# Performance work log

Measured on AMD Instinct MI355X. Metric: run time of the kernel, lower is better.

## Reference

```python
import jax, jax.numpy as jnp
import numpy as np

D_STATE = 11
DT_RANK = 4
BN_EPS = 1e-5
RMS_EPS = 1e-5


def setup_inputs() -> dict:
    key = jax.random.key(0)
    ks = jax.random.split(key, 8)
    B, L, D = 8, 8192, 64
    x = jax.random.normal(ks[0], (B, L, D), dtype=jnp.float32)
    tconv_w = jax.random.normal(ks[1], (64, 1, 63), dtype=jnp.float32) * 0.1
    bn_gamma = jnp.ones((64,), jnp.float32)
    bn_beta = jnp.zeros((64,), jnp.float32)
    x_proj_weight = jax.random.normal(ks[2], (1, DT_RANK + 2 * D_STATE, 64), jnp.float32) * (64 ** -0.5)
    dt_projs_weight = jax.random.uniform(ks[3], (1, 64, DT_RANK), jnp.float32, -0.5, 0.5)
    # dt bias ~ inverse-softplus of dt in [1e-3, 1e-1]
    dt = jnp.exp(jax.random.uniform(ks[4], (1, 64), jnp.float32) * (np.log(0.1) - np.log(0.001)) + np.log(0.001))
    dt_projs_bias = dt + jnp.log(-jnp.expm1(-dt))
    A_logs = jnp.log(jnp.broadcast_to(jnp.arange(1, D_STATE + 1, dtype=jnp.float32), (64, D_STATE)))
    Ds = jnp.ones((64,), jnp.float32)
    rms_scale = jnp.ones((1, 64), jnp.float32)
    return {"x": x, "tconv_w": tconv_w, "bn_gamma": bn_gamma, "bn_beta": bn_beta,
            "x_proj_weight": x_proj_weight, "dt_projs_weight": dt_projs_weight,
            "dt_projs_bias": dt_projs_bias, "A_logs": A_logs, "Ds": Ds,
            "rms_scale": rms_scale}


def _silu(v):
    return v * jax.nn.sigmoid(v)


def reference(x, tconv_w, bn_gamma, bn_beta, x_proj_weight, dt_projs_weight,
              dt_projs_bias, A_logs, Ds, rms_scale):
    B, L, D = x.shape  # D == 64
    z = x
    xc = jnp.transpose(x, (0, 2, 1))  # (B, C, L)

    # depthwise conv1d, kernel 63, pad 31, no bias
    xc = jax.lax.conv_general_dilated(
        xc, tconv_w, window_strides=(1,), padding=[(31, 31)],
        feature_group_count=D, dimension_numbers=("NCH", "OIH", "NCH"))

    # BatchNorm1d (training-mode forward: batch stats, biased variance)
    mean = jnp.mean(xc, axis=(0, 2), keepdims=True)
    var = jnp.mean((xc - mean) ** 2, axis=(0, 2), keepdims=True)
    xc = (xc - mean) / jnp.sqrt(var + BN_EPS) * bn_gamma[None, :, None] + bn_beta[None, :, None]

    u = _silu(xc)  # (B, d_inner, L)

    # x_proj: (B,d,L) x (C,d) -> (B,C,L)
    x_dbl = jnp.einsum("bdl,cd->bcl", u, x_proj_weight[0])
    dts = x_dbl[:, :DT_RANK]                      # (B, r, L)
    Bs = x_dbl[:, DT_RANK:DT_RANK + D_STATE]      # (B, N, L)
    Cs = x_dbl[:, DT_RANK + D_STATE:]             # (B, N, L)

    dts = jnp.einsum("brl,dr->bdl", dts, dt_projs_weight[0])
    delta = jax.nn.softplus(dts + dt_projs_bias[0][None, :, None])  # (B,d,L)

    A = -jnp.exp(A_logs)  # (d, N)
    dA = jnp.exp(jnp.einsum("bdl,dn->lbdn", delta, A))      # (L,B,d,N)
    dBu = jnp.einsum("bdl,bnl->lbdn", delta * u, Bs)        # (L,B,d,N)

    def step(h, inp):
        dA_t, dBu_t = inp
        h = dA_t * h + dBu_t
        return h, h

    h0 = jnp.zeros((B, u.shape[1], D_STATE), dtype=u.dtype)
    _, hs = jax.lax.scan(step, h0, (dA, dBu))  # (L,B,d,N)

    y = jnp.einsum("lbdn,bnl->bdl", hs, Cs) + Ds[None, :, None] * u  # (B,d,L)

    y = jnp.transpose(y, (0, 2, 1))  # (B, L, d_inner)

    # RMSNorm
    ms = jnp.mean(y ** 2, axis=-1, keepdims=True)
    y = (rms_scale / jnp.sqrt(ms + RMS_EPS)) * y

    out = y * _silu(z)
    return out
```

## Files before the change

kernel.cpp:

```cpp
#include <hip/hip_runtime.h>
#include <hip/hip_bf16.h>
#include <hip/hip_fp16.h>
#include <math.h>

#define NB 8
#define LL 8192
#define DD 64
#define NS 11
#define NR 4
#define NC 512
#define LC (LL/NC)
#define CONV_LT 128
#define KW 63
#define PJ 64
#define NBKT 64
#define UH 72
#define WH 72

typedef _Float16 h2v __attribute__((ext_vector_type(2)));

__device__ __forceinline__ float sigmoidf_(float v){ return 1.f/(1.f+__expf(-v)); }
__device__ __forceinline__ float rnd16(float v){ return __half2float(__float2half_rn(v)); }

__global__ void k_zero(float* __restrict__ p){
  p[blockIdx.x*256 + threadIdx.x] = 0.f;
}

__global__ __launch_bounds__(512,4) void k_conv(const float* __restrict__ x,
                                              const float* __restrict__ w,
                                              __half* __restrict__ xc,
                                              __half* __restrict__ gate,
                                              float* __restrict__ bn_acc){
  const int b  = blockIdx.x / (LL/CONV_LT);
  const int lt = blockIdx.x % (LL/CONV_LT);
  const int l0 = lt*CONV_LT;
  __shared__ float xt[(CONV_LT+62)*DD];
  __shared__ float rs[512], rq[512];
  const int t = threadIdx.x;
  for (int i=t; i<(CONV_LT+62)*DD; i+=512){
    int lrel = i/DD, d = i%DD;
    int lg = l0 - 31 + lrel;
    xt[i] = (lg>=0 && lg<LL) ? x[((size_t)b*LL+lg)*DD + d] : 0.f;
  }
  __syncthreads();
  const int d = t & 63;
  const int base = (t >> 6) * 16;
  float acc[16];
  #pragma unroll
  for (int j=0;j<16;j++) acc[j]=0.f;
  #pragma unroll 1
  for (int kb=0; kb<4; ++kb){
    float wv[16];
    #pragma unroll
    for (int kk=0;kk<16;kk++){
      int k = kb*16+kk;
      wv[kk] = (k<KW) ? w[d*KW+k] : 0.f;
    }
    float xw[31];
    #pragma unroll
    for (int i=0;i<31;i++) xw[i] = xt[(base+kb*16+i)*DD + d];
    #pragma unroll
    for (int j=0;j<16;j++){
      #pragma unroll
      for (int kk=0;kk<16;kk++){
        acc[j] = fmaf(wv[kk], xw[j+kk], acc[j]);
      }
    }
  }
  float lsum=0.f, lsq=0.f;
  #pragma unroll
  for (int j=0;j<16;j++){
    size_t p = (size_t)b*LL + l0+base+j;
    xc[p*DD + d] = __float2half_rn(acc[j]);
    float z = xt[(base+j+31)*DD + d];
    gate[p*DD + d] = __float2half_rn(z * sigmoidf_(z));
    lsum += acc[j]; lsq = fmaf(acc[j],acc[j],lsq);
  }
  rs[t]=lsum; rq[t]=lsq;
  __syncthreads();
  if (t<64){
    float s=0.f, q=0.f;
    #pragma unroll
    for (int g=0; g<8; ++g){ s += rs[t+64*g]; q += rq[t+64*g]; }
    const int bkt = (blockIdx.x & (NBKT-1))*128;
    atomicAdd(&bn_acc[bkt+t],    s);
    atomicAdd(&bn_acc[bkt+64+t], q);
  }
}

__global__ __launch_bounds__(256,5) void k_proj(const __half* __restrict__ xc,
                                              const float* __restrict__ bn_acc,
                                              const float* __restrict__ gamma,
                                              const float* __restrict__ beta,
                                              const float* __restrict__ xpw,
                                              const float* __restrict__ dtw,
                                              const float* __restrict__ dtb,
                                              const float* __restrict__ Alog,
                                              __half2* __restrict__ duo,
                                              __half* __restrict__ bch,
                                              float* __restrict__ chunkst){
  const int b  = blockIdx.x / (LL/PJ);
  const int lt = blockIdx.x % (LL/PJ);
  const int l0 = lt*PJ;
  __shared__ __align__(16) _Float16 ulh[PJ*UH];
  __shared__ __align__(16) _Float16 wshh[26*WH];
  __shared__ float bcl[PJ][24];
  __shared__ float xd[PJ*NR];
  __shared__ float dtwsh[64*NR];
  __shared__ float bnred[2][4][64];
  const int t = threadIdx.x;
  for (int i=t; i<26*64; i+=256){ int c=i>>6, dd=i&63; wshh[c*WH+dd] = (_Float16)xpw[i]; }
  dtwsh[t] = dtw[t];
  if (t < 128){ bcl[t>>1][(t&1)?23:11] = 0.f; }
  const int d = t & 63, wv = t >> 6;
  {
    float ms=0.f, qs=0.f;
    #pragma unroll
    for (int k=wv*16; k<wv*16+16; ++k){
      ms += bn_acc[k*128 + d];
      qs += bn_acc[k*128 + 64 + d];
    }
    bnred[0][wv][d]=ms; bnred[1][wv][d]=qs;
  }
  __syncthreads();
  float msum = bnred[0][0][d]+bnred[0][1][d]+bnred[0][2][d]+bnred[0][3][d];
  float qsum = bnred[1][0][d]+bnred[1][1][d]+bnred[1][2][d]+bnred[1][3][d];
  const float inv_n = 1.f/((float)NB*(float)LL);
  float mean = msum*inv_n;
  float var  = qsum*inv_n - mean*mean;
  float sc = gamma[d] * rsqrtf(var + 1e-5f);
  float sh = beta[d] - mean*sc;
  float uu[16];
  #pragma unroll
  for (int j=0;j<16;j++){
    int lr = wv*16 + j;
    float v = __half2float(xc[((size_t)b*LL + l0+lr)*DD + d]);
    v = fmaf(v, sc, sh);
    _Float16 uh = (_Float16)(v * sigmoidf_(v));
    uu[j] = (float)uh;
    ulh[lr*UH+d] = uh;
  }
  __syncthreads();
  {
    const int cp  = t & 15;
    const int lrb = t >> 4;
    if (cp < 13){
      float acc0[4] = {0.f,0.f,0.f,0.f};
      float acc1[4] = {0.f,0.f,0.f,0.f};
      #pragma unroll 2
      for (int dd8=0; dd8<8; ++dd8){
        float4 w0v = *reinterpret_cast<const float4*>(&wshh[(2*cp  )*WH + dd8*8]);
        float4 w1v = *reinterpret_cast<const float4*>(&wshh[(2*cp+1)*WH + dd8*8]);
        const h2v* w0 = reinterpret_cast<const h2v*>(&w0v);
        const h2v* w1 = reinterpret_cast<const h2v*>(&w1v);
        #pragma unroll
        for (int p=0;p<4;p++){
          float4 uvv = *reinterpret_cast<const float4*>(&ulh[(lrb*4+p)*UH + dd8*8]);
          const h2v* up = reinterpret_cast<const h2v*>(&uvv);
#if __has_builtin(__builtin_amdgcn_fdot2)
          acc0[p] = __builtin_amdgcn_fdot2(w0[0], up[0], acc0[p], false);
          acc0[p] = __builtin_amdgcn_fdot2(w0[1], up[1], acc0[p], false);
          acc0[p] = __builtin_amdgcn_fdot2(w0[2], up[2], acc0[p], false);
          acc0[p] = __builtin_amdgcn_fdot2(w0[3], up[3], acc0[p], false);
          acc1[p] = __builtin_amdgcn_fdot2(w1[0], up[0], acc1[p], false);
          acc1[p] = __builtin_amdgcn_fdot2(w1[1], up[1], acc1[p], false);
          acc1[p] = __builtin_amdgcn_fdot2(w1[2], up[2], acc1[p], false);
          acc1[p] = __builtin_amdgcn_fdot2(w1[3], up[3], acc1[p], false);
#else
          #pragma unroll
          for (int q2=0;q2<4;q2++){
            acc0[p] += (float)w0[q2][0]*(float)up[q2][0] + (float)w0[q2][1]*(float)up[q2][1];
            acc1[p] += (float)w1[q2][0]*(float)up[q2][0] + (float)w1[q2][1]*(float)up[q2][1];
          }
#endif
        }
      }
      #pragma unroll
      for (int cc=0; cc<2; ++cc){
        int c = 2*cp+cc;
        #pragma unroll
        for (int p=0;p<4;p++){
          int lr = lrb*4+p;
          float v = cc ? acc1[p] : acc0[p];
          if (c < NR) xd[lr*NR+c] = v;
          else {
            int pos = c - NR;
            int slot = (pos < NS) ? pos : pos+1;
            bcl[lr][slot] = rnd16(v);
          }
        }
      }
    }
  }
  __syncthreads();
  {
    __half2* dst = reinterpret_cast<__half2*>(bch + ((size_t)b*LL + l0)*24);
    #pragma unroll
    for (int r=0;r<3;r++){
      int j = t + 256*r;
      int pos = j / 12, sl = (j % 12)*2;
      dst[j] = __floats2half2_rn(bcl[pos][sl], bcl[pos][sl+1]);
    }
  }
  {
    const float bias = dtb[d];
    const float dw0 = dtwsh[d*NR+0], dw1 = dtwsh[d*NR+1],
                dw2 = dtwsh[d*NR+2], dw3 = dtwsh[d*NR+3];
    float a0 = -__expf(Alog[d*NS]);
    bool fast = true;
    #pragma unroll
    for (int n=1;n<NS;n++){
      float an = -__expf(Alog[d*NS+n]);
      fast = fast && (fabsf(an - (float)(n+1)*a0) <= 1e-4f*(float)(n+1));
    }
    const int task = b*NC + lt*4 + wv;
    float h[12];
    #pragma unroll
    for (int n=0;n<12;n++) h[n]=0.f;
    float dsum=0.f;
    #pragma unroll 4
    for (int l=0;l<LC;++l){
      int lr = wv*LC + l;
      float4 xv = *reinterpret_cast<const float4*>(&xd[lr*NR]);
      float s = fmaf(dw0,xv.x, fmaf(dw1,xv.y, fmaf(dw2,xv.z, fmaf(dw3,xv.w, bias))));
      float de = rnd16(fmaxf(s,0.f) + __logf(1.f + __expf(-fabsf(s))));
      float u_ = uu[l];
      float du = de*u_;
      dsum += de;
      duo[((size_t)b*LL + l0+lr)*DD + d] = __floats2half2_rn(de, u_);
      float bca[12];
      const float4* q = reinterpret_cast<const float4*>(&bcl[lr][0]);
      *reinterpret_cast<float4*>(&bca[0]) = q[0];
      *reinterpret_cast<float4*>(&bca[4]) = q[1];
      *reinterpret_cast<float4*>(&bca[8]) = q[2];
      if (fast){
        float r = __expf(a0*de);
        float dA = 1.f;
        #pragma unroll
        for (int n=0;n<NS;n++){
          dA *= r;
          h[n] = fmaf(dA, h[n], du*bca[n]);
        }
      } else {
        #pragma unroll
        for (int n=0;n<NS;n++){
          float dA = __expf(-__expf(Alog[d*NS+n])*de);
          h[n] = fmaf(dA, h[n], du*bca[n]);
        }
      }
    }
    h[11] = dsum;
    float4* o = reinterpret_cast<float4*>(chunkst + ((size_t)task*64 + d)*12);
    o[0] = *reinterpret_cast<float4*>(&h[0]);
    o[1] = *reinterpret_cast<float4*>(&h[4]);
    o[2] = *reinterpret_cast<float4*>(&h[8]);
  }
}

__global__ __launch_bounds__(64) void k_scanMid(const float* __restrict__ chunkst,
                                                const float* __restrict__ Alog,
                                                __half* __restrict__ hin){
  const int wid  = blockIdx.x;
  const int lane = threadIdx.x & 63;
  const int b = wid >> 6, d = wid & 63;
  const int c0 = lane*8;
  const size_t recbase = (((size_t)b*NC + c0)*64 + d)*12;
  float rec[8][12];
  #pragma unroll
  for (int j=0;j<8;j++){
    const float4* q = reinterpret_cast<const float4*>(chunkst + recbase + (size_t)j*768);
    *reinterpret_cast<float4*>(&rec[j][0]) = q[0];
    *reinterpret_cast<float4*>(&rec[j][4]) = q[1];
    *reinterpret_cast<float4*>(&rec[j][8]) = q[2];
  }
  float aAll[NS];
  #pragma unroll
  for (int n=0;n<NS;n++) aAll[n] = -expf(Alog[d*NS+n]);
  bool fast = true;
  #pragma unroll
  for (int n=1;n<NS;n++)
    fast = fast && (fabsf(aAll[n] - (float)(n+1)*aAll[0]) <= 1e-4f*(float)(n+1));
  float Aa[NS], Bb[NS];
  #pragma unroll
  for (int n=0;n<NS;n++){ Aa[n]=1.f; Bb[n]=0.f; }
  #pragma unroll
  for (int j=0;j<8;j++){
    float ds = rec[j][11];
    if (fast){
      float r = __expf(aAll[0]*ds);
      float dA = 1.f;
      #pragma unroll
      for (int n=0;n<NS;n++){
        dA *= r;
        Bb[n] = fmaf(dA, Bb[n], rec[j][n]);
        Aa[n] *= dA;
      }
    } else {
      #pragma unroll
      for (int n=0;n<NS;n++){
        float dA = __expf(aAll[n]*ds);
        Bb[n] = fmaf(dA, Bb[n], rec[j][n]);
        Aa[n] *= dA;
      }
    }
  }
  #pragma unroll
  for (int n=0;n<NS;n++){
    float A = Aa[n], Bv = Bb[n];
    #pragma unroll
    for (int off=1; off<64; off<<=1){
      float Ap=__shfl_up(A,off,64), Bp=__shfl_up(Bv,off,64);
      if (lane>=off){ Bv = fmaf(A,Bp,Bv); A*=Ap; }
    }
    float hs = __shfl_up(Bv,1,64);
    Bb[n] = (lane==0) ? 0.f : hs;
  }
  #pragma unroll
  for (int j=0;j<8;j++){
    float ds = rec[j][11];
    float outv[12];
    if (fast){
      float r = __expf(aAll[0]*ds);
      float dA = 1.f;
      #pragma unroll
      for (int n=0;n<NS;n++){
        outv[n] = Bb[n];
        dA *= r;
        Bb[n] = fmaf(dA, Bb[n], rec[j][n]);
      }
    } else {
      #pragma unroll
      for (int n=0;n<NS;n++){
        outv[n] = Bb[n];
        float dA = __expf(aAll[n]*ds);
        Bb[n] = fmaf(dA, Bb[n], rec[j][n]);
      }
    }
    __half2 oh[8];
    oh[0]=__floats2half2_rn(outv[0],outv[1]);
    oh[1]=__floats2half2_rn(outv[2],outv[3]);
    oh[2]=__floats2half2_rn(outv[4],outv[5]);
    oh[3]=__floats2half2_rn(outv[6],outv[7]);
    oh[4]=__floats2half2_rn(outv[8],outv[9]);
    oh[5]=__floats2half2_rn(outv[10],0.f);
    oh[6]=__floats2half2_rn(0.f,0.f);
    oh[7]=oh[6];
    float4* o = reinterpret_cast<float4*>(hin + (((size_t)b*NC + c0+j)*64 + d)*16);
    o[0] = *reinterpret_cast<float4*>(&oh[0]);
    o[1] = *reinterpret_cast<float4*>(&oh[4]);
  }
}

__global__ __launch_bounds__(256,4) void k_scanB(const __half2* __restrict__ duo,
                                               const __half* __restrict__ bch,
                                               const float* __restrict__ Alog,
                                               const __half* __restrict__ hin,
                                               const float* __restrict__ Dsv,
                                               const float* __restrict__ rmss,
                                               const __half* __restrict__ gate,
                                               float* __restrict__ out){
  const int task = blockIdx.x*4 + (threadIdx.x>>6);
  const int d = threadIdx.x & 63;
  const int b = task / NC, c = task % NC;
  float a0 = -expf(Alog[d*NS]);
  bool fast = true;
  #pragma unroll
  for (int n=1;n<NS;n++){
    float an = -expf(Alog[d*NS+n]);
    fast = fast && (fabsf(an - (float)(n+1)*a0) <= 1e-4f*(float)(n+1));
  }
  float h[12];
  {
    const float4* q = reinterpret_cast<const float4*>(hin + ((size_t)task*64 + d)*16);
    float4 r0 = q[0], r1 = q[1];
    __half2 hh[8];
    *reinterpret_cast<float4*>(&hh[0]) = r0;
    *reinterpret_cast<float4*>(&hh[4]) = r1;
    h[0]=__low2float(hh[0]);  h[1]=__high2float(hh[0]);
    h[2]=__low2float(hh[1]);  h[3]=__high2float(hh[1]);
    h[4]=__low2float(hh[2]);  h[5]=__high2float(hh[2]);
    h[6]=__low2float(hh[3]);  h[7]=__high2float(hh[3]);
    h[8]=__low2float(hh[4]);  h[9]=__high2float(hh[4]);
    h[10]=__low2float(hh[5]); h[11]=0.f;
  }
  const float Dd = Dsv[d];
  const float rsc = rmss[d];
  const int l0 = c*LC;
  #pragma unroll 1
  for (int g=0; g<LC/4; ++g){
    __half2 dv[4];
    float4 bq0[4], bq1[4], bq2[4];
    __half gz[4];
    #pragma unroll
    for (int i=0;i<4;i++){
      size_t p = (size_t)b*LL + l0 + g*4 + i;
      dv[i] = duo[p*DD+d];
      const float4* q = reinterpret_cast<const float4*>(bch + p*24);
      bq0[i]=q[0]; bq1[i]=q[1]; bq2[i]=q[2];
      gz[i] = gate[p*DD+d];
    }
    #pragma unroll
    for (int i=0;i<4;i++){
      size_t p = (size_t)b*LL + l0 + g*4 + i;
      float de = __low2float(dv[i]), uu = __high2float(dv[i]);
      float du = de*uu;
      __half2 h2[12];
      *reinterpret_cast<float4*>(&h2[0]) = bq0[i];
      *reinterpret_cast<float4*>(&h2[4]) = bq1[i];
      *reinterpret_cast<float4*>(&h2[8]) = bq2[i];
      float y = Dd*uu;
      if (fast){
        float r = __expf(a0*de);
        float dA = 1.f;
        #pragma unroll
        for (int n=0;n<NS;n++){
          dA *= r;
          float bn = (n&1) ? __high2float(h2[n>>1]) : __low2float(h2[n>>1]);
          float cn = (n&1) ? __high2float(h2[(12+n)>>1]) : __low2float(h2[(12+n)>>1]);
          h[n] = fmaf(dA, h[n], du*bn);
          y = fmaf(h[n], cn, y);
        }
      } else {
        #pragma unroll
        for (int n=0;n<NS;n++){
          float dA = __expf(-expf(Alog[d*NS+n])*de);
          float bn = (n&1) ? __high2float(h2[n>>1]) : __low2float(h2[n>>1]);
          float cn = (n&1) ? __high2float(h2[(12+n)>>1]) : __low2float(h2[(12+n)>>1]);
          h[n] = fmaf(dA, h[n], du*bn);
          y = fmaf(h[n], cn, y);
        }
      }
      float ss = y*y;
      #pragma unroll
      for (int m=1;m<64;m<<=1) ss += __shfl_xor(ss, m, 64);
      float yn = rsc * rsqrtf(ss*(1.f/64.f) + 1e-5f) * y;
      out[p*DD+d] = yn * __half2float(gz[i]);
    }
  }
}

extern "C" void kernel_launch(void* const* d_in, const int* in_sizes, int n_in,
                              void* d_out, int out_size, void* d_ws, size_t ws_size,
                              hipStream_t stream) {
  const float* x     = (const float*)d_in[0];
  const float* w     = (const float*)d_in[1];
  const float* gamma = (const float*)d_in[2];
  const float* beta  = (const float*)d_in[3];
  const float* xpw   = (const float*)d_in[4];
  const float* dtw   = (const float*)d_in[5];
  const float* dtb   = (const float*)d_in[6];
  const float* Alog  = (const float*)d_in[7];
  const float* Dsv   = (const float*)d_in[8];
  const float* rmss  = (const float*)d_in[9];
  float* out = (float*)d_out;

  float* f = (float*)d_ws;
  const size_t n_xld = (size_t)NB*LL*DD;
  __half*  xc   = (__half*)f;
  __half*  gate = xc + n_xld;
  __half2* duo  = (__half2*)(f + n_xld);
  __half*  bch  = (__half*)(f + 2*n_xld);
  float* chunkst = f + 2*n_xld + (size_t)NB*LL*24/2 + 1024;
  __half* hin   = (__half*)(chunkst + (size_t)NB*NC*64*12);
  float* bn_acc = chunkst + (size_t)NB*NC*64*12 + (size_t)NB*NC*64*8;

  k_zero   <<<NBKT*128/256, 256, 0, stream>>>(bn_acc);
  k_conv   <<<NB*(LL/CONV_LT), 512, 0, stream>>>(x, w, xc, gate, bn_acc);
  k_proj   <<<NB*(LL/PJ), 256, 0, stream>>>(xc, bn_acc, gamma, beta, xpw, dtw, dtb, Alog, duo, bch, chunkst);
  k_scanMid<<<NB*DD, 64, 0, stream>>>(chunkst, Alog, hin);
  k_scanB  <<<(NB*NC)/4, 256, 0, stream>>>(duo, bch, Alog, hin, Dsv, rmss, gate, out);
}
```

Before: 80.85 us.

## Replace BN atomics with per-block partials and split chunk-state scan across two waves

```diff
diff --git a/kernel.cpp b/kernel.cpp
--- a/kernel.cpp
+++ b/kernel.cpp
@@ -13,24 +13,20 @@
 #define CONV_LT 128
 #define KW 63
 #define PJ 64
-#define NBKT 64
 #define UH 72
 #define WH 72
+#define NCB (NB*(LL/CONV_LT))
 
 typedef _Float16 h2v __attribute__((ext_vector_type(2)));
 
 __device__ __forceinline__ float sigmoidf_(float v){ return 1.f/(1.f+__expf(-v)); }
 __device__ __forceinline__ float rnd16(float v){ return __half2float(__float2half_rn(v)); }
-
-__global__ void k_zero(float* __restrict__ p){
-  p[blockIdx.x*256 + threadIdx.x] = 0.f;
-}
 
 __global__ __launch_bounds__(512,4) void k_conv(const float* __restrict__ x,
                                               const float* __restrict__ w,
                                               __half* __restrict__ xc,
                                               __half* __restrict__ gate,
-                                              float* __restrict__ bn_acc){
+                                              float* __restrict__ bn_part){
   const int b  = blockIdx.x / (LL/CONV_LT);
   const int lt = blockIdx.x % (LL/CONV_LT);
   const int l0 = lt*CONV_LT;
@@ -82,16 +78,41 @@
     float s=0.f, q=0.f;
     #pragma unroll
     for (int g=0; g<8; ++g){ s += rs[t+64*g]; q += rq[t+64*g]; }
-    const int bkt = (blockIdx.x & (NBKT-1))*128;
-    atomicAdd(&bn_acc[bkt+t],    s);
-    atomicAdd(&bn_acc[bkt+64+t], q);
+    bn_part[(size_t)blockIdx.x*128 + t]      = s;
+    bn_part[(size_t)blockIdx.x*128 + 64 + t] = q;
+  }
+}
+
+__global__ __launch_bounds__(512) void k_bnred(const float* __restrict__ bn_part,
+                                               const float* __restrict__ gamma,
+                                               const float* __restrict__ beta,
+                                               float* __restrict__ bnp){
+  __shared__ float red[2][8][64];
+  const int t = threadIdx.x;
+  const int d = t & 63, grp = t >> 6;
+  float s=0.f, q=0.f;
+  #pragma unroll 8
+  for (int k=grp*64; k<grp*64+64; ++k){
+    s += bn_part[(size_t)k*128 + d];
+    q += bn_part[(size_t)k*128 + 64 + d];
+  }
+  red[0][grp][d]=s; red[1][grp][d]=q;
+  __syncthreads();
+  if (t < 64){
+    float ms=0.f, qs=0.f;
+    #pragma unroll
+    for (int g=0;g<8;g++){ ms += red[0][g][t]; qs += red[1][g][t]; }
+    const float inv_n = 1.f/((float)NB*(float)LL);
+    float mean = ms*inv_n;
+    float var  = qs*inv_n - mean*mean;
+    float sc = gamma[t] * rsqrtf(var + 1e-5f);
+    bnp[t]    = sc;
+    bnp[64+t] = beta[t] - mean*sc;
   }
 }
 
 __global__ __launch_bounds__(256,5) void k_proj(const __half* __restrict__ xc,
-                                              const float* __restrict__ bn_acc,
-                                              const float* __restrict__ gamma,
-                                              const float* __restrict__ beta,
+                                              const float* __restrict__ bnp,
                                               const float* __restrict__ xpw,
                                               const float* __restrict__ dtw,
                                               const float* __restrict__ dtb,
@@ -107,29 +128,12 @@
   __shared__ float bcl[PJ][24];
   __shared__ float xd[PJ*NR];
   __shared__ float dtwsh[64*NR];
-  __shared__ float bnred[2][4][64];
   const int t = threadIdx.x;
   for (int i=t; i<26*64; i+=256){ int c=i>>6, dd=i&63; wshh[c*WH+dd] = (_Float16)xpw[i]; }
   dtwsh[t] = dtw[t];
   if (t < 128){ bcl[t>>1][(t&1)?23:11] = 0.f; }
   const int d = t & 63, wv = t >> 6;
-  {
-    float ms=0.f, qs=0.f;
-    #pragma unroll
-    for (int k=wv*16; k<wv*16+16; ++k){
-      ms += bn_acc[k*128 + d];
-      qs += bn_acc[k*128 + 64 + d];
-    }
-    bnred[0][wv][d]=ms; bnred[1][wv][d]=qs;
-  }
-  __syncthreads();
-  float msum = bnred[0][0][d]+bnred[0][1][d]+bnred[0][2][d]+bnred[0][3][d];
-  float qsum = bnred[1][0][d]+bnred[1][1][d]+bnred[1][2][d]+bnred[1][3][d];
-  const float inv_n = 1.f/((float)NB*(float)LL);
-  float mean = msum*inv_n;
-  float var  = qsum*inv_n - mean*mean;
-  float sc = gamma[d] * rsqrtf(var + 1e-5f);
-  float sh = beta[d] - mean*sc;
+  float sc = bnp[d], sh = bnp[64+d];
   float uu[16];
   #pragma unroll
   for (int j=0;j<16;j++){
@@ -257,18 +261,19 @@
   }
 }
 
-__global__ __launch_bounds__(64) void k_scanMid(const float* __restrict__ chunkst,
-                                                const float* __restrict__ Alog,
-                                                __half* __restrict__ hin){
+__global__ __launch_bounds__(128) void k_scanMid(const float* __restrict__ chunkst,
+                                                 const float* __restrict__ Alog,
+                                                 __half* __restrict__ hin){
   const int wid  = blockIdx.x;
+  const int wave = threadIdx.x >> 6;
   const int lane = threadIdx.x & 63;
   const int b = wid >> 6, d = wid & 63;
-  const int c0 = lane*8;
-  const size_t recbase = (((size_t)b*NC + c0)*64 + d)*12;
-  float rec[8][12];
-  #pragma unroll
-  for (int j=0;j<8;j++){
-    const float4* q = reinterpret_cast<const float4*>(chunkst + recbase + (size_t)j*768);
+  const int cbase = wave*256 + lane*4;
+  __shared__ float wtot[2][12];
+  float rec[4][12];
+  #pragma unroll
+  for (int j=0;j<4;j++){
+    const float4* q = reinterpret_cast<const float4*>(chunkst + (((size_t)b*NC + cbase+j)*64 + d)*12);
     *reinterpret_cast<float4*>(&rec[j][0]) = q[0];
     *reinterpret_cast<float4*>(&rec[j][4]) = q[1];
     *reinterpret_cast<float4*>(&rec[j][8]) = q[2];
@@ -280,11 +285,11 @@
   #pragma unroll
   for (int n=1;n<NS;n++)
     fast = fast && (fabsf(aAll[n] - (float)(n+1)*aAll[0]) <= 1e-4f*(float)(n+1));
-  float Aa[NS], Bb[NS];
-  #pragma unroll
-  for (int n=0;n<NS;n++){ Aa[n]=1.f; Bb[n]=0.f; }
-  #pragma unroll
-  for (int j=0;j<8;j++){
+  float Ai[NS], Bi[NS];
+  #pragma unroll
+  for (int n=0;n<NS;n++){ Ai[n]=1.f; Bi[n]=0.f; }
+  #pragma unroll
+  for (int j=0;j<4;j++){
     float ds = rec[j][11];
     if (fast){
       float r = __expf(aAll[0]*ds);
@@ -292,62 +297,72 @@
       #pragma unroll
       for (int n=0;n<NS;n++){
         dA *= r;
-        Bb[n] = fmaf(dA, Bb[n], rec[j][n]);
-        Aa[n] *= dA;
+        Bi[n] = fmaf(dA, Bi[n], rec[j][n]);
+        Ai[n] *= dA;
       }
     } else {
       #pragma unroll
       for (int n=0;n<NS;n++){
         float dA = __expf(aAll[n]*ds);
-        Bb[n] = fmaf(dA, Bb[n], rec[j][n]);
-        Aa[n] *= dA;
+        Bi[n] = fmaf(dA, Bi[n], rec[j][n]);
+        Ai[n] *= dA;
       }
     }
   }
   #pragma unroll
   for (int n=0;n<NS;n++){
-    float A = Aa[n], Bv = Bb[n];
+    float A = Ai[n], Bv = Bi[n];
     #pragma unroll
     for (int off=1; off<64; off<<=1){
       float Ap=__shfl_up(A,off,64), Bp=__shfl_up(Bv,off,64);
       if (lane>=off){ Bv = fmaf(A,Bp,Bv); A*=Ap; }
     }
-    float hs = __shfl_up(Bv,1,64);
-    Bb[n] = (lane==0) ? 0.f : hs;
-  }
-  #pragma unroll
-  for (int j=0;j<8;j++){
+    Ai[n]=A; Bi[n]=Bv;
+  }
+  if (wave==0 && lane==63){
+    #pragma unroll
+    for (int n=0;n<NS;n++){ wtot[0][n]=Ai[n]; wtot[1][n]=Bi[n]; }
+  }
+  __syncthreads();
+  float hst[NS];
+  #pragma unroll
+  for (int n=0;n<NS;n++){
+    float Aex = __shfl_up(Ai[n],1,64);
+    float Bex = __shfl_up(Bi[n],1,64);
+    if (lane==0){ Aex=1.f; Bex=0.f; }
+    if (wave==0) hst[n] = Bex;
+    else         hst[n] = fmaf(Aex, wtot[1][n], Bex);
+  }
+  #pragma unroll
+  for (int j=0;j<4;j++){
     float ds = rec[j][11];
-    float outv[12];
+    __half2 oh[8];
+    oh[0]=__floats2half2_rn(hst[0],hst[1]);
+    oh[1]=__floats2half2_rn(hst[2],hst[3]);
+    oh[2]=__floats2half2_rn(hst[4],hst[5]);
+    oh[3]=__floats2half2_rn(hst[6],hst[7]);
+    oh[4]=__floats2half2_rn(hst[8],hst[9]);
+    oh[5]=__floats2half2_rn(hst[10],0.f);
+    oh[6]=__floats2half2_rn(0.f,0.f);
+    oh[7]=oh[6];
+    float4* o = reinterpret_cast<float4*>(hin + (((size_t)b*NC + cbase+j)*64 + d)*16);
+    o[0] = *reinterpret_cast<float4*>(&oh[0]);
+    o[1] = *reinterpret_cast<float4*>(&oh[4]);
     if (fast){
       float r = __expf(aAll[0]*ds);
       float dA = 1.f;
       #pragma unroll
       for (int n=0;n<NS;n++){
-        outv[n] = Bb[n];
         dA *= r;
-        Bb[n] = fmaf(dA, Bb[n], rec[j][n]);
+        hst[n] = fmaf(dA, hst[n], rec[j][n]);
       }
     } else {
       #pragma unroll
       for (int n=0;n<NS;n++){
-        outv[n] = Bb[n];
         float dA = __expf(aAll[n]*ds);
-        Bb[n] = fmaf(dA, Bb[n], rec[j][n]);
-      }
-    }
-    __half2 oh[8];
-    oh[0]=__floats2half2_rn(outv[0],outv[1]);
-    oh[1]=__floats2half2_rn(outv[2],outv[3]);
-    oh[2]=__floats2half2_rn(outv[4],outv[5]);
-    oh[3]=__floats2half2_rn(outv[6],outv[7]);
-    oh[4]=__floats2half2_rn(outv[8],outv[9]);
-    oh[5]=__floats2half2_rn(outv[10],0.f);
-    oh[6]=__floats2half2_rn(0.f,0.f);
-    oh[7]=oh[6];
-    float4* o = reinterpret_cast<float4*>(hin + (((size_t)b*NC + c0+j)*64 + d)*16);
-    o[0] = *reinterpret_cast<float4*>(&oh[0]);
-    o[1] = *reinterpret_cast<float4*>(&oh[4]);
+        hst[n] = fmaf(dA, hst[n], rec[j][n]);
+      }
+    }
   }
 }
 
@@ -462,11 +477,12 @@
   __half*  bch  = (__half*)(f + 2*n_xld);
   float* chunkst = f + 2*n_xld + (size_t)NB*LL*24/2 + 1024;
   __half* hin   = (__half*)(chunkst + (size_t)NB*NC*64*12);
-  float* bn_acc = chunkst + (size_t)NB*NC*64*12 + (size_t)NB*NC*64*8;
-
-  k_zero   <<<NBKT*128/256, 256, 0, stream>>>(bn_acc);
-  k_conv   <<<NB*(LL/CONV_LT), 512, 0, stream>>>(x, w, xc, gate, bn_acc);
-  k_proj   <<<NB*(LL/PJ), 256, 0, stream>>>(xc, bn_acc, gamma, beta, xpw, dtw, dtb, Alog, duo, bch, chunkst);
-  k_scanMid<<<NB*DD, 64, 0, stream>>>(chunkst, Alog, hin);
+  float* bn_part = chunkst + (size_t)NB*NC*64*12 + (size_t)NB*NC*64*8;
+  float* bnp     = bn_part + (size_t)NCB*128;
+
+  k_conv   <<<NCB, 512, 0, stream>>>(x, w, xc, gate, bn_part);
+  k_bnred  <<<1, 512, 0, stream>>>(bn_part, gamma, beta, bnp);
+  k_proj   <<<NB*(LL/PJ), 256, 0, stream>>>(xc, bnp, xpw, dtw, dtb, Alog, duo, bch, chunkst);
+  k_scanMid<<<NB*DD, 128, 0, stream>>>(chunkst, Alog, hin);
   k_scanB  <<<(NB*NC)/4, 256, 0, stream>>>(duo, bch, Alog, hin, Dsv, rmss, gate, out);
 }
```

Result: no change. 80.06 us, median of 2 (-1.0%).
